# Optimization experiments

Measured on AMD Instinct MI355X. Metric: run time of the kernel, lower is better.

## Reference

```python
import jax, jax.numpy as jnp
import numpy as np

N_NODES = 50000
N_EDGES = 500000
IN_DIM = 128
H1, C1 = 4, 64   # layer1: heads=4, out=64, concat -> 256
H2, C2 = 1, 64   # layer2: heads=1, out=64


def setup_inputs() -> dict:
    key = jax.random.key(0)
    ks = jax.random.split(key, 16)
    p = lambda k, shp: (jax.random.normal(k, shp, dtype=jnp.float32) * 0.1)
    return {
        "x": jax.random.normal(ks[0], (N_NODES, IN_DIM), dtype=jnp.float32),
        "edge_index": jax.random.randint(ks[1], (2, N_EDGES), 0, N_NODES, dtype=jnp.int32),
        "edge_attr": jax.random.uniform(ks[2], (N_EDGES, 1), dtype=jnp.float32),
        # layer 1 params
        "W1": p(ks[3], (IN_DIM, H1 * C1)),
        "We1": p(ks[4], (1, H1 * C1)),
        "as1": p(ks[5], (H1, C1)),
        "ad1": p(ks[6], (H1, C1)),
        "ae1": p(ks[7], (H1, C1)),
        "b1": jnp.zeros((H1 * C1,), dtype=jnp.float32),
        # layer 2 params
        "W2": p(ks[8], (H1 * C1, H2 * C2)),
        "We2": p(ks[9], (1, H2 * C2)),
        "as2": p(ks[10], (H2, C2)),
        "ad2": p(ks[11], (H2, C2)),
        "ae2": p(ks[12], (H2, C2)),
        "b2": jnp.zeros((H2 * C2,), dtype=jnp.float32),
    }


def _add_self_loops(src, dst, edge_attr, n):
    # PyG fill_value='mean': loop edge_attr = mean of incoming edge attrs per node
    cnt = jax.ops.segment_sum(jnp.ones((src.shape[0],), edge_attr.dtype), dst, num_segments=n)
    loop_attr = jax.ops.segment_sum(edge_attr, dst, num_segments=n) / jnp.maximum(cnt, 1.0)[:, None]
    idx = jnp.arange(n, dtype=src.dtype)
    return (jnp.concatenate([src, idx]), jnp.concatenate([dst, idx]),
            jnp.concatenate([edge_attr, loop_attr], axis=0))


def _gat_conv(x, src, dst, edge_attr, W, We, a_src, a_dst, a_edge, bias, heads, out_ch):
    n = x.shape[0]
    h = (x @ W).reshape(n, heads, out_ch)                      # [N,H,C]
    e = (edge_attr @ We).reshape(-1, heads, out_ch)            # [E,H,C]
    alpha = ((h * a_src).sum(-1)[src]                          # gather src score
             + (h * a_dst).sum(-1)[dst]                        # gather dst score
             + (e * a_edge).sum(-1))                           # [E,H]
    alpha = jax.nn.leaky_relu(alpha, 0.2)
    m = jax.ops.segment_max(alpha, dst, num_segments=n)        # per-target max
    alpha = jnp.exp(alpha - m[dst])
    denom = jax.ops.segment_sum(alpha, dst, num_segments=n)
    alpha = alpha / (denom[dst] + 1e-16)
    out = jax.ops.segment_sum(h[src] * alpha[..., None], dst, num_segments=n)
    return out.reshape(n, heads * out_ch) + bias


def reference(x, edge_index, edge_attr, W1, We1, as1, ad1, ae1, b1,
              W2, We2, as2, ad2, ae2, b2):
    src, dst = edge_index[0], edge_index[1]
    src, dst, ea = _add_self_loops(src, dst, edge_attr, x.shape[0])
    h = jax.nn.elu(_gat_conv(x, src, dst, ea, W1, We1, as1, ad1, ae1, b1, H1, C1))
    return _gat_conv(h, src, dst, ea, W2, We2, as2, ad2, ae2, b2, H2, C2)
```

## Files before the change

kernel.cpp:

```cpp
#include <hip/hip_runtime.h>
#include <math.h>

#define NN 50000
#define NE 500000
#define DIM 128
#define HC1 256
#define HC2 64
#define BCAP 64
#define NBUCKET ((NE + 255) / 256)

typedef __attribute__((ext_vector_type(8))) short short8;
typedef __attribute__((ext_vector_type(4))) float floatx4;


__device__ __forceinline__ unsigned short f2bf(float f) {
  unsigned int u = __float_as_uint(f);
  unsigned int r = (u + 0x7FFFu + ((u >> 16) & 1u)) >> 16;
  return (unsigned short)r;
}
__device__ __forceinline__ float bf2f(unsigned short s) {
  return __uint_as_float(((unsigned int)s) << 16);
}

__device__ __forceinline__ float waveReduce(float v) {
  v += __shfl_down(v, 32);
  v += __shfl_down(v, 16);
  v += __shfl_down(v, 8);
  v += __shfl_down(v, 4);
  v += __shfl_down(v, 2);
  v += __shfl_down(v, 1);
  return v;
}

__device__ __forceinline__ void decodeP(unsigned long long p, int& cn, float& lea) {
  int c = (int)(p >> 40);
  cn = (c < BCAP) ? c : BCAP;
  float asum = (float)(p & 0xFFFFFFFFFFULL) * (1.0f / 16777216.0f);
  lea = asum / fmaxf((float)c, 1.0f);
}


__global__ __launch_bounds__(256) void k_build(const int* __restrict__ src,
                                               const int* __restrict__ dst,
                                               const float* __restrict__ ea,
                                               unsigned long long* __restrict__ P,
                                               unsigned int* __restrict__ ebuf,
                                               const float* __restrict__ W1,
                                               const float* __restrict__ W2,
                                               const float* __restrict__ We1,
                                               const float* __restrict__ ae1,
                                               const float* __restrict__ We2,
                                               const float* __restrict__ ae2,
                                               unsigned short* __restrict__ W1T,
                                               unsigned short* __restrict__ W2T,
                                               float* __restrict__ ce) {
  int b = blockIdx.x, t = threadIdx.x;
  if (b < NBUCKET) {
    int e = b * 256 + t;
    if (e < NE) {
      int d = dst[e];
      float eav = ea[e];
      unsigned long long fx = (unsigned long long)(unsigned int)__float2uint_rn(eav * 16777216.0f);
      unsigned long long old = atomicAdd(&P[d], (1ULL << 40) | fx);
      int pos = (int)(old >> 40);
      unsigned int ea16 = __float2uint_rn(eav * 65536.0f);
      if (ea16 > 65535u) ea16 = 65535u;
      if (pos < BCAP)
        ebuf[d * BCAP + pos] = (ea16 << 16) | (unsigned int)src[e];
    }
  } else if (b < NBUCKET + 128) {
    int idx = (b - NBUCKET) * 256 + t;
    int n = idx >> 7, k = idx & 127;
    W1T[idx] = f2bf(W1[k * 256 + n]);
  } else if (b < NBUCKET + 192) {
    int idx = (b - NBUCKET - 128) * 256 + t;
    int n = idx >> 8, k = idx & 255;
    W2T[idx] = f2bf(W2[k * 64 + n]);
  } else {
    int h = t >> 6, lane = t & 63;
    float p = We1[h * 64 + lane] * ae1[h * 64 + lane];
    p = waveReduce(p);
    if (lane == 0) ce[h] = p;
    if (h == 0) {
      float q = We2[lane] * ae2[lane];
      q = waveReduce(q);
      if (lane == 0) ce[4] = q;
    }
  }
}


__global__ __launch_bounds__(256) void k_gemm1m(const float* __restrict__ x,
                                                const unsigned short* __restrict__ W1T,
                                                const float* __restrict__ as1,
                                                const float* __restrict__ ad1,
                                                unsigned short* __restrict__ h1b,
                                                float* __restrict__ ss1,
                                                float* __restrict__ sd1) {
  __shared__ unsigned short As[64 * 136];
  int t = threadIdx.x;
  int wave = t >> 6, lane = t & 63;
  int q = lane >> 4, ln = lane & 15;
  int m0 = blockIdx.x * 64;
  int n0 = wave * 64;

  short8 bfr[4][4];
#pragma unroll
  for (int c = 0; c < 4; c++)
#pragma unroll
    for (int ks = 0; ks < 4; ks++)
      bfr[c][ks] = *(const short8*)&W1T[(n0 + c * 16 + ln) * 128 + ks * 32 + q * 8];

#pragma unroll
  for (int rep = 0; rep < 8; rep++) {
    int chunk = t + 256 * rep;
    int m = chunk >> 5, kk = (chunk & 31) * 4;
    int gr = m0 + m;
    float4 v = (gr < NN) ? *(const float4*)&x[gr * DIM + kk]
                         : make_float4(0.f, 0.f, 0.f, 0.f);
    ushort4 o;
    o.x = f2bf(v.x); o.y = f2bf(v.y); o.z = f2bf(v.z); o.w = f2bf(v.w);
    *(ushort4*)&As[m * 136 + kk] = o;
  }
  __syncthreads();

  floatx4 acc[4][4];
#pragma unroll
  for (int r = 0; r < 4; r++)
#pragma unroll
    for (int c = 0; c < 4; c++) acc[r][c] = (floatx4){0.f, 0.f, 0.f, 0.f};

#pragma unroll
  for (int ks = 0; ks < 4; ks++) {
    short8 afr[4];
#pragma unroll
    for (int r = 0; r < 4; r++)
      afr[r] = *(const short8*)&As[(r * 16 + ln) * 136 + ks * 32 + q * 8];
#pragma unroll
    for (int r = 0; r < 4; r++)
#pragma unroll
      for (int c = 0; c < 4; c++)
        acc[r][c] = __builtin_amdgcn_mfma_f32_16x16x32_bf16(afr[r], bfr[c][ks], acc[r][c], 0, 0, 0);
  }

  float as1v[4], ad1v[4];
#pragma unroll
  for (int c = 0; c < 4; c++) {
    as1v[c] = as1[n0 + c * 16 + ln];
    ad1v[c] = ad1[n0 + c * 16 + ln];
  }

#pragma unroll
  for (int r = 0; r < 4; r++) {
#pragma unroll
    for (int i = 0; i < 4; i++) {
      int gm = m0 + r * 16 + q * 4 + i;
      if (gm < NN) {
#pragma unroll
        for (int c = 0; c < 4; c++)
          h1b[gm * HC1 + n0 + c * 16 + ln] = f2bf(acc[r][c][i]);
      }
      float ps = acc[r][0][i] * as1v[0];
      float pd = acc[r][0][i] * ad1v[0];
#pragma unroll
      for (int c = 1; c < 4; c++) {
        ps = fmaf(acc[r][c][i], as1v[c], ps);
        pd = fmaf(acc[r][c][i], ad1v[c], pd);
      }
#pragma unroll
      for (int m = 1; m < 16; m <<= 1) {
        ps += __shfl_xor(ps, m);
        pd += __shfl_xor(pd, m);
      }
      if (ln == 0 && gm < NN) {
        ss1[gm * 4 + wave] = ps;
        sd1[gm * 4 + wave] = pd;
      }
    }
  }
}

__global__ __launch_bounds__(256) void k_gemm2m(const unsigned short* __restrict__ out1b,
                                                const unsigned short* __restrict__ W2T,
                                                const float* __restrict__ as2,
                                                const float* __restrict__ ad2,
                                                unsigned short* __restrict__ h2b,
                                                float* __restrict__ ss2,
                                                float* __restrict__ sd2) {
  __shared__ unsigned short As[64 * 264];
  __shared__ float ssp[4][64], sdp[4][64];
  int t = threadIdx.x;
  int wave = t >> 6, lane = t & 63;
  int q = lane >> 4, ln = lane & 15;
  int m0 = blockIdx.x * 64;
  int n0 = wave * 16;

  short8 bfr[8];
#pragma unroll
  for (int ks = 0; ks < 8; ks++)
    bfr[ks] = *(const short8*)&W2T[(n0 + ln) * 256 + ks * 32 + q * 8];

  short8 zero8 = {0, 0, 0, 0, 0, 0, 0, 0};
#pragma unroll
  for (int rep = 0; rep < 8; rep++) {
    int chunk = t + 256 * rep;
    int m = chunk >> 5, kk = (chunk & 31) * 8;
    int gr = m0 + m;
    short8 vv = (gr < NN) ? *(const short8*)&out1b[gr * 256 + kk] : zero8;
    *(short8*)&As[m * 264 + kk] = vv;
  }
  __syncthreads();

  floatx4 acc[4];
#pragma unroll
  for (int r = 0; r < 4; r++) acc[r] = (floatx4){0.f, 0.f, 0.f, 0.f};

#pragma unroll
  for (int ks = 0; ks < 8; ks++) {
#pragma unroll
    for (int r = 0; r < 4; r++) {
      short8 afr = *(const short8*)&As[(r * 16 + ln) * 264 + ks * 32 + q * 8];
      acc[r] = __builtin_amdgcn_mfma_f32_16x16x32_bf16(afr, bfr[ks], acc[r], 0, 0, 0);
    }
  }

  float as2v = as2[n0 + ln], ad2v = ad2[n0 + ln];
#pragma unroll
  for (int r = 0; r < 4; r++) {
#pragma unroll
    for (int i = 0; i < 4; i++) {
      int gm = m0 + r * 16 + q * 4 + i;
      if (gm < NN) h2b[gm * HC2 + n0 + ln] = f2bf(acc[r][i]);
      float ps = acc[r][i] * as2v;
      float pd = acc[r][i] * ad2v;
#pragma unroll
      for (int m = 1; m < 16; m <<= 1) {
        ps += __shfl_xor(ps, m);
        pd += __shfl_xor(pd, m);
      }
      if (ln == 0) {
        ssp[wave][r * 16 + q * 4 + i] = ps;
        sdp[wave][r * 16 + q * 4 + i] = pd;
      }
    }
  }
  __syncthreads();
  if (t < 64) {
    int gm = m0 + t;
    if (gm < NN) {
      ss2[gm] = ssp[0][t] + ssp[1][t] + ssp[2][t] + ssp[3][t];
      sd2[gm] = sdp[0][t] + sdp[1][t] + sdp[2][t] + sdp[3][t];
    }
  }
}


__global__ __launch_bounds__(256) void k_agg1(const unsigned short* __restrict__ h1b,
                                              const unsigned long long* __restrict__ P,
                                              const unsigned int* __restrict__ ebuf,
                                              const float* __restrict__ ss1,
                                              const float* __restrict__ sd1,
                                              const float* __restrict__ ce,
                                              const float* __restrict__ b1,
                                              unsigned short* __restrict__ out1b) {
  int v = (blockIdx.x * blockDim.x + threadIdx.x) >> 6;
  int lane = threadIdx.x & 63;
  int h = lane >> 4;
  int c4 = lane * 4;
  int l16 = lane & 15;
  int vu = __builtin_amdgcn_readfirstlane(v);
  int cn; float lea;
  decodeP(P[vu], cn, lea);
  cn = __builtin_amdgcn_readfirstlane(cn);
  int beg = vu * BCAP;
  int end = beg + cn;
  float sdh = sd1[vu * 4 + h];
  float ceh = ce[h];
  float4 acc = make_float4(0.f, 0.f, 0.f, 0.f);
  float l = 0.f;

  for (int base = beg; base < end; base += 16) {
    unsigned int meta = ebuf[base + l16];
#pragma unroll
    for (int b4 = 0; b4 < 4; b4++) {
      if (base + b4 * 4 >= end) break;
      float ssv[4], ea4[4];
      ushort4 u[4];
      bool vld[4];
#pragma unroll
      for (int jj = 0; jj < 4; jj++) {
        int j = b4 * 4 + jj;
        bool val = (base + j < end);
        unsigned int m = __builtin_amdgcn_readlane(meta, j);
        int sj = val ? (int)(m & 0xFFFFu) : 0;
        ea4[jj] = (float)(m >> 16) * (1.0f / 65536.0f);
        vld[jj] = val;
        ssv[jj] = ss1[sj * 4 + h];
        u[jj] = *(const ushort4*)&h1b[sj * HC1 + c4];
      }
#pragma unroll
      for (int jj = 0; jj < 4; jj++) {
        float x = fmaf(ea4[jj], ceh, ssv[jj] + sdh);
        x = fmaxf(x, 0.2f * x);
        float a = vld[jj] ? __expf(x) : 0.f;
        l += a;
        acc.x = fmaf(a, bf2f(u[jj].x), acc.x);
        acc.y = fmaf(a, bf2f(u[jj].y), acc.y);
        acc.z = fmaf(a, bf2f(u[jj].z), acc.z);
        acc.w = fmaf(a, bf2f(u[jj].w), acc.w);
      }
    }
  }
  {
    float x = fmaf(lea, ceh, ss1[vu * 4 + h] + sdh);
    x = fmaxf(x, 0.2f * x);
    float a = __expf(x);
    ushort4 u = *(const ushort4*)&h1b[vu * HC1 + c4];
    l += a;
    acc.x = fmaf(a, bf2f(u.x), acc.x);
    acc.y = fmaf(a, bf2f(u.y), acc.y);
    acc.z = fmaf(a, bf2f(u.z), acc.z);
    acc.w = fmaf(a, bf2f(u.w), acc.w);
  }
  float inv = 1.f / (l + 1e-16f);
  float4 bv = *(const float4*)&b1[c4];
  float4 o;
  o.x = acc.x * inv + bv.x;
  o.y = acc.y * inv + bv.y;
  o.z = acc.z * inv + bv.z;
  o.w = acc.w * inv + bv.w;
  o.x = (o.x > 0.f) ? o.x : expm1f(o.x);
  o.y = (o.y > 0.f) ? o.y : expm1f(o.y);
  o.z = (o.z > 0.f) ? o.z : expm1f(o.z);
  o.w = (o.w > 0.f) ? o.w : expm1f(o.w);
  ushort4 ob;
  ob.x = f2bf(o.x); ob.y = f2bf(o.y); ob.z = f2bf(o.z); ob.w = f2bf(o.w);
  *(ushort4*)&out1b[vu * HC1 + c4] = ob;
}

__global__ __launch_bounds__(256) void k_agg2(const unsigned short* __restrict__ h2b,
                                              const unsigned long long* __restrict__ P,
                                              const unsigned int* __restrict__ ebuf,
                                              const float* __restrict__ ss2,
                                              const float* __restrict__ sd2,
                                              const float* __restrict__ ce,
                                              const float* __restrict__ b2,
                                              float* __restrict__ out) {
  int v = (blockIdx.x * blockDim.x + threadIdx.x) >> 6;
  int lane = threadIdx.x & 63;
  int g = lane >> 4;
  int c = lane & 15;
  int l16 = lane & 15;
  int vu = __builtin_amdgcn_readfirstlane(v);
  int cn; float lea;
  decodeP(P[vu], cn, lea);
  cn = __builtin_amdgcn_readfirstlane(cn);
  int beg = vu * BCAP;
  int end = beg + cn;
  float sdv = sd2[vu];
  float cev = ce[4];
  float4 acc = make_float4(0.f, 0.f, 0.f, 0.f);
  float l = 0.f;

  for (int base = beg; base < end; base += 16) {
    int nb = end - base;
    unsigned int meta = ebuf[base + l16];
    float ssv[4], eav[4];
    bool vld[4];
    ushort4 u[4];
#pragma unroll
    for (int sub = 0; sub < 4; sub++) {
      int j = sub * 4 + g;
      bool val = (j < nb);
      unsigned int m = (unsigned int)__shfl((int)meta, j);
      int sj = val ? (int)(m & 0xFFFFu) : 0;
      eav[sub] = (float)(m >> 16) * (1.0f / 65536.0f);
      vld[sub] = val;
      ssv[sub] = ss2[sj];
      u[sub] = *(const ushort4*)&h2b[sj * HC2 + c * 4];
    }
#pragma unroll
    for (int sub = 0; sub < 4; sub++) {
      float x = fmaf(eav[sub], cev, ssv[sub] + sdv);
      x = fmaxf(x, 0.2f * x);
      float a = vld[sub] ? __expf(x) : 0.f;
      l += a;
      acc.x = fmaf(a, bf2f(u[sub].x), acc.x);
      acc.y = fmaf(a, bf2f(u[sub].y), acc.y);
      acc.z = fmaf(a, bf2f(u[sub].z), acc.z);
      acc.w = fmaf(a, bf2f(u[sub].w), acc.w);
    }
  }
#pragma unroll
  for (int m = 16; m <= 32; m <<= 1) {
    acc.x += __shfl_xor(acc.x, m);
    acc.y += __shfl_xor(acc.y, m);
    acc.z += __shfl_xor(acc.z, m);
    acc.w += __shfl_xor(acc.w, m);
    l += __shfl_xor(l, m);
  }
  {
    float x = fmaf(lea, cev, ss2[vu] + sdv);
    x = fmaxf(x, 0.2f * x);
    float a = __expf(x);
    ushort4 us = *(const ushort4*)&h2b[vu * HC2 + c * 4];
    l += a;
    acc.x = fmaf(a, bf2f(us.x), acc.x);
    acc.y = fmaf(a, bf2f(us.y), acc.y);
    acc.z = fmaf(a, bf2f(us.z), acc.z);
    acc.w = fmaf(a, bf2f(us.w), acc.w);
  }
  if (g == 0) {
    float inv = 1.f / (l + 1e-16f);
    float4 bv = *(const float4*)&b2[c * 4];
    float4 o;
    o.x = acc.x * inv + bv.x;
    o.y = acc.y * inv + bv.y;
    o.z = acc.z * inv + bv.z;
    o.w = acc.w * inv + bv.w;
    *(float4*)&out[vu * HC2 + c * 4] = o;
  }
}


extern "C" void kernel_launch(void* const* d_in, const int* in_sizes, int n_in,
                              void* d_out, int out_size, void* d_ws, size_t ws_size,
                              hipStream_t stream) {
  const float* x   = (const float*)d_in[0];
  const int*   ei  = (const int*)d_in[1];
  const float* ea  = (const float*)d_in[2];
  const float* W1  = (const float*)d_in[3];
  const float* We1 = (const float*)d_in[4];
  const float* as1 = (const float*)d_in[5];
  const float* ad1 = (const float*)d_in[6];
  const float* ae1 = (const float*)d_in[7];
  const float* b1  = (const float*)d_in[8];
  const float* W2  = (const float*)d_in[9];
  const float* We2 = (const float*)d_in[10];
  const float* as2 = (const float*)d_in[11];
  const float* ad2 = (const float*)d_in[12];
  const float* ae2 = (const float*)d_in[13];
  const float* b2  = (const float*)d_in[14];
  const int* srcp = ei;
  const int* dstp = ei + NE;

  char* w = (char*)d_ws;
  unsigned long long* P = (unsigned long long*)(w + 0);
  float* ce      = (float*)(w + 400064);
  float* ss1     = (float*)(w + 400576);
  float* sd1     = (float*)(w + 1200576);
  float* ss2     = (float*)(w + 2000576);
  float* sd2     = (float*)(w + 2200576);
  unsigned int* ebuf = (unsigned int*)(w + 2400640);
  unsigned short* h1b   = (unsigned short*)(w + 15200640);
  unsigned short* out1b = (unsigned short*)(w + 40800640);
  unsigned short* h2b   = (unsigned short*)(w + 66400640);
  unsigned short* W1T   = (unsigned short*)(w + 72800640);
  unsigned short* W2T   = (unsigned short*)(w + 72866176);

  hipMemsetAsync(w, 0, 400000, stream);

  k_build<<<NBUCKET + 193, 256, 0, stream>>>(srcp, dstp, ea, P, ebuf,
                                             W1, W2, We1, ae1, We2, ae2,
                                             W1T, W2T, ce);

  k_gemm1m<<<(NN + 63) / 64, 256, 0, stream>>>(x, W1T, as1, ad1, h1b, ss1, sd1);
  k_agg1<<<(NN * 64 + 255) / 256, 256, 0, stream>>>(h1b, P, ebuf, ss1, sd1, ce, b1, out1b);

  k_gemm2m<<<(NN + 63) / 64, 256, 0, stream>>>(out1b, W2T, as2, ad2, h2b, ss2, sd2);
  k_agg2<<<(NN * 64 + 255) / 256, 256, 0, stream>>>(h2b, P, ebuf, ss2, sd2, ce, b2,
                                                    (float*)d_out);
}
```

Before: 232.0 us.

## Fuse edge-bucket build into layer-1 GEMM launch to overlap atomics with MFMA

Moves the edge scatter (atomic count and attr sum into P, ebuf fill) out of the build kernel and into the same grid as the layer-1 GEMM, using the first NBUCKET blocks for edges and the rest for GEMM tiles. Weight transpose and edge constant prep stay in a small separate kernel launched first. The aim is to overlap the atomic-heavy, latency-bound edge scatter with the compute-bound GEMM and to remove the serialization between them. The cost is an extra small launch. The GEMM blocks also carry the shared-memory allocation even for edge blocks, which can reduce occupancy for the scatter part.

```diff
diff --git a/kernel.cpp b/kernel.cpp
--- a/kernel.cpp
+++ b/kernel.cpp
@@ -8,6 +8,7 @@
 #define HC2 64
 #define BCAP 64
 #define NBUCKET ((NE + 255) / 256)
+#define GB ((NN + 63) / 64)
 
 typedef __attribute__((ext_vector_type(8))) short short8;
 typedef __attribute__((ext_vector_type(4))) float floatx4;
@@ -40,40 +41,22 @@
 }
 
 
-__global__ __launch_bounds__(256) void k_build(const int* __restrict__ src,
-                                               const int* __restrict__ dst,
-                                               const float* __restrict__ ea,
-                                               unsigned long long* __restrict__ P,
-                                               unsigned int* __restrict__ ebuf,
-                                               const float* __restrict__ W1,
-                                               const float* __restrict__ W2,
-                                               const float* __restrict__ We1,
-                                               const float* __restrict__ ae1,
-                                               const float* __restrict__ We2,
-                                               const float* __restrict__ ae2,
-                                               unsigned short* __restrict__ W1T,
-                                               unsigned short* __restrict__ W2T,
-                                               float* __restrict__ ce) {
+__global__ __launch_bounds__(256) void k_prep(const float* __restrict__ W1,
+                                              const float* __restrict__ W2,
+                                              const float* __restrict__ We1,
+                                              const float* __restrict__ ae1,
+                                              const float* __restrict__ We2,
+                                              const float* __restrict__ ae2,
+                                              unsigned short* __restrict__ W1T,
+                                              unsigned short* __restrict__ W2T,
+                                              float* __restrict__ ce) {
   int b = blockIdx.x, t = threadIdx.x;
-  if (b < NBUCKET) {
-    int e = b * 256 + t;
-    if (e < NE) {
-      int d = dst[e];
-      float eav = ea[e];
-      unsigned long long fx = (unsigned long long)(unsigned int)__float2uint_rn(eav * 16777216.0f);
-      unsigned long long old = atomicAdd(&P[d], (1ULL << 40) | fx);
-      int pos = (int)(old >> 40);
-      unsigned int ea16 = __float2uint_rn(eav * 65536.0f);
-      if (ea16 > 65535u) ea16 = 65535u;
-      if (pos < BCAP)
-        ebuf[d * BCAP + pos] = (ea16 << 16) | (unsigned int)src[e];
-    }
-  } else if (b < NBUCKET + 128) {
-    int idx = (b - NBUCKET) * 256 + t;
+  if (b < 128) {
+    int idx = b * 256 + t;
     int n = idx >> 7, k = idx & 127;
     W1T[idx] = f2bf(W1[k * 256 + n]);
-  } else if (b < NBUCKET + 192) {
-    int idx = (b - NBUCKET - 128) * 256 + t;
+  } else if (b < 192) {
+    int idx = (b - 128) * 256 + t;
     int n = idx >> 8, k = idx & 255;
     W2T[idx] = f2bf(W2[k * 64 + n]);
   } else {
@@ -90,18 +73,40 @@
 }
 
 
-__global__ __launch_bounds__(256) void k_gemm1m(const float* __restrict__ x,
-                                                const unsigned short* __restrict__ W1T,
-                                                const float* __restrict__ as1,
-                                                const float* __restrict__ ad1,
-                                                unsigned short* __restrict__ h1b,
-                                                float* __restrict__ ss1,
-                                                float* __restrict__ sd1) {
+__global__ __launch_bounds__(256) void k_fused(const int* __restrict__ src,
+                                               const int* __restrict__ dst,
+                                               const float* __restrict__ ea,
+                                               unsigned long long* __restrict__ P,
+                                               unsigned int* __restrict__ ebuf,
+                                               const float* __restrict__ x,
+                                               const unsigned short* __restrict__ W1T,
+                                               const float* __restrict__ as1,
+                                               const float* __restrict__ ad1,
+                                               unsigned short* __restrict__ h1b,
+                                               float* __restrict__ ss1,
+                                               float* __restrict__ sd1) {
   __shared__ unsigned short As[64 * 136];
   int t = threadIdx.x;
+
+  if (blockIdx.x < NBUCKET) {
+    int e = blockIdx.x * 256 + t;
+    if (e < NE) {
+      int d = dst[e];
+      float eav = ea[e];
+      unsigned long long fx = (unsigned long long)(unsigned int)__float2uint_rn(eav * 16777216.0f);
+      unsigned long long old = atomicAdd(&P[d], (1ULL << 40) | fx);
+      int pos = (int)(old >> 40);
+      unsigned int ea16 = __float2uint_rn(eav * 65536.0f);
+      if (ea16 > 65535u) ea16 = 65535u;
+      if (pos < BCAP)
+        ebuf[d * BCAP + pos] = (ea16 << 16) | (unsigned int)src[e];
+    }
+    return;
+  }
+
   int wave = t >> 6, lane = t & 63;
   int q = lane >> 4, ln = lane & 15;
-  int m0 = blockIdx.x * 64;
+  int m0 = (blockIdx.x - NBUCKET) * 64;
   int n0 = wave * 64;
 
   short8 bfr[4][4];
@@ -460,11 +465,10 @@
 
   hipMemsetAsync(w, 0, 400000, stream);
 
-  k_build<<<NBUCKET + 193, 256, 0, stream>>>(srcp, dstp, ea, P, ebuf,
-                                             W1, W2, We1, ae1, We2, ae2,
-                                             W1T, W2T, ce);
-
-  k_gemm1m<<<(NN + 63) / 64, 256, 0, stream>>>(x, W1T, as1, ad1, h1b, ss1, sd1);
+  k_prep<<<193, 256, 0, stream>>>(W1, W2, We1, ae1, We2, ae2, W1T, W2T, ce);
+  k_fused<<<NBUCKET + GB, 256, 0, stream>>>(srcp, dstp, ea, P, ebuf,
+                                            x, W1T, as1, ad1, h1b, ss1, sd1);
+
   k_agg1<<<(NN * 64 + 255) / 256, 256, 0, stream>>>(h1b, P, ebuf, ss1, sd1, ce, b1, out1b);
 
   k_gemm2m<<<(NN + 63) / 64, 256, 0, stream>>>(out1b, W2T, as2, ad2, h2b, ss2, sd2);
```

Result: faster. 226.0 us (-2.6%).
